# Performance work log

Measured on AMD Instinct MI355X. Metric: run time of the kernel, lower is better.

The kernel has to match this reference:

```python
import jax, jax.numpy as jnp
import numpy as np

B, TE, TD, DE, DD = 4, 256, 256, 512, 512


def setup_inputs() -> dict:
    key = jax.random.key(0)
    k1, k2, k3, k4, k5 = jax.random.split(key, 5)
    return {
        "encoder_outputs": jax.random.normal(k1, (B, TE, DE), dtype=jnp.float32),
        "decoder_outputs": jax.random.normal(k2, (B, TD, DD), dtype=jnp.float32),
        "U_a": jax.random.normal(k3, (DE, DE), dtype=jnp.float32) * 0.05,
        "W_a": jax.random.normal(k4, (DD, DE), dtype=jnp.float32) * 0.05,
        "V_a": jax.random.normal(k5, (DE,), dtype=jnp.float32) * 0.05,
    }


def reference(encoder_outputs, decoder_outputs, U_a, W_a, V_a):
    # U_a_dot_h: [B, Te, De] -- precomputed once, as in the original
    Uh = jnp.einsum("bec,cd->bed", encoder_outputs, U_a)
    # W_a_dot_s for all decoder steps at once (original loops over t): [B, Td, De]
    Ws = jnp.einsum("btc,cd->btd", decoder_outputs, W_a)
    # additive energies: tanh(Uh + Ws) . V_a -> [B, Td, Te]
    e = jnp.einsum("bted,d->bte", jnp.tanh(Uh[:, None, :, :] + Ws[:, :, None, :]), V_a)
    attn = jax.nn.softmax(e, axis=-1)  # softmax over encoder timesteps
    # context: weighted sum of encoder outputs -> [B, Td, De]
    context = jnp.einsum("bte,bec->btc", attn, encoder_outputs)
    return context, attn
```

## Files before the change

kernel.cpp:

```cpp
#include <hip/hip_runtime.h>

#define B_    4
#define TE_   256
#define TD_   256
#define DE_   512
#define K_    512

typedef __attribute__((ext_vector_type(8))) short bf16x8;
typedef __attribute__((ext_vector_type(4))) float f32x4;

#define C1F 2.8853900817779268f

__device__ __forceinline__ ushort f2bf(float x) {
  uint u = __float_as_uint(x);
  return (ushort)((u + 0x7fffu + ((u >> 16) & 1u)) >> 16);
}
__device__ __forceinline__ float bf2f(ushort h) {
  return __uint_as_float(((uint)h) << 16);
}
__device__ __forceinline__ float exp2_fast(float x) {
  float r;
  asm("v_exp_f32 %0, %1" : "=v"(r) : "v"(x));
  return r;
}

__global__ __launch_bounds__(256) void conv_hilo(
    const float* __restrict__ enc, const float* __restrict__ dec,
    ushort* __restrict__ ehi, ushort* __restrict__ elo,
    ushort* __restrict__ dhi, ushort* __restrict__ dlo) {
  const float* in = blockIdx.y ? dec : enc;
  ushort* hi = blockIdx.y ? dhi : ehi;
  ushort* lo = blockIdx.y ? dlo : elo;
  int i = (blockIdx.x * 256 + threadIdx.x) * 4;
  float4 v = *(const float4*)&in[i];
  ushort4 h, l;
  h.x = f2bf(v.x); l.x = f2bf(v.x - bf2f(h.x));
  h.y = f2bf(v.y); l.y = f2bf(v.y - bf2f(h.y));
  h.z = f2bf(v.z); l.z = f2bf(v.z - bf2f(h.z));
  h.w = f2bf(v.w); l.w = f2bf(v.w - bf2f(h.w));
  *(ushort4*)&hi[i] = h;
  *(ushort4*)&lo[i] = l;
}

__global__ __launch_bounds__(256) void conv_bt(
    const float* __restrict__ Ua, const float* __restrict__ Wa,
    ushort* __restrict__ uhi, ushort* __restrict__ ulo,
    ushort* __restrict__ whi, ushort* __restrict__ wlo) {
  const float* in = blockIdx.z ? Wa : Ua;
  ushort* thi = blockIdx.z ? whi : uhi;
  ushort* tlo = blockIdx.z ? wlo : ulo;
  __shared__ float tile[64][65];
  int k0 = blockIdx.y * 64, n0 = blockIdx.x * 64;
  int tid = threadIdx.x;
#pragma unroll
  for (int i = 0; i < 16; ++i) {
    int idx = tid + i * 256;
    int r = idx >> 6, c = idx & 63;
    tile[r][c] = in[(size_t)(k0 + r) * 512 + n0 + c];
  }
  __syncthreads();
#pragma unroll
  for (int i = 0; i < 16; ++i) {
    int idx = tid + i * 256;
    int rn = idx >> 6, ck = idx & 63;
    float x = tile[ck][rn] * C1F;
    ushort h = f2bf(x);
    size_t o = (size_t)(n0 + rn) * 512 + k0 + ck;
    thi[o] = h;
    tlo[o] = f2bf(x - bf2f(h));
  }
}

__global__ __launch_bounds__(64) void gemm_mfma(
    const ushort* __restrict__ ehi, const ushort* __restrict__ elo,
    const ushort* __restrict__ dhi, const ushort* __restrict__ dlo,
    const ushort* __restrict__ uhi, const ushort* __restrict__ ulo,
    const ushort* __restrict__ whi, const ushort* __restrict__ wlo,
    float* __restrict__ UhT, float* __restrict__ Ws) {
  const ushort *Ahi, *Alo, *Bhi, *Blo;
  int bid = blockIdx.x, bm, bn;
  if (blockIdx.z == 0) {
    Ahi = uhi; Alo = ulo; Bhi = ehi; Blo = elo;
    bn = (bid & 31) * 32; bm = (bid >> 5) * 32;
  } else {
    Ahi = dhi; Alo = dlo; Bhi = whi; Blo = wlo;
    bn = (bid & 15) * 32; bm = (bid >> 4) * 32;
  }
  int lane = threadIdx.x;
  int frow = lane & 15, fk = (lane >> 4) * 8;
  size_t ao = (size_t)(bm + frow) * K_ + fk;
  size_t bo = (size_t)(bn + frow) * K_ + fk;
  const ushort* pah0 = Ahi + ao; const ushort* pah1 = pah0 + 16 * K_;
  const ushort* pal0 = Alo + ao; const ushort* pal1 = pal0 + 16 * K_;
  const ushort* pbh0 = Bhi + bo; const ushort* pbh1 = pbh0 + 16 * K_;
  const ushort* pbl0 = Blo + bo; const ushort* pbl1 = pbl0 + 16 * K_;
  f32x4 a00 = {}, a01 = {}, a10 = {}, a11 = {};
#pragma unroll 2
  for (int k0 = 0; k0 < K_; k0 += 32) {
    bf16x8 ah0 = *(const bf16x8*)&pah0[k0], ah1 = *(const bf16x8*)&pah1[k0];
    bf16x8 al0 = *(const bf16x8*)&pal0[k0], al1 = *(const bf16x8*)&pal1[k0];
    bf16x8 bh0 = *(const bf16x8*)&pbh0[k0], bh1 = *(const bf16x8*)&pbh1[k0];
    bf16x8 bl0 = *(const bf16x8*)&pbl0[k0], bl1 = *(const bf16x8*)&pbl1[k0];
    a00 = __builtin_amdgcn_mfma_f32_16x16x32_bf16(ah0, bh0, a00, 0, 0, 0);
    a01 = __builtin_amdgcn_mfma_f32_16x16x32_bf16(ah0, bh1, a01, 0, 0, 0);
    a10 = __builtin_amdgcn_mfma_f32_16x16x32_bf16(ah1, bh0, a10, 0, 0, 0);
    a11 = __builtin_amdgcn_mfma_f32_16x16x32_bf16(ah1, bh1, a11, 0, 0, 0);
    a00 = __builtin_amdgcn_mfma_f32_16x16x32_bf16(ah0, bl0, a00, 0, 0, 0);
    a01 = __builtin_amdgcn_mfma_f32_16x16x32_bf16(ah0, bl1, a01, 0, 0, 0);
    a10 = __builtin_amdgcn_mfma_f32_16x16x32_bf16(ah1, bl0, a10, 0, 0, 0);
    a11 = __builtin_amdgcn_mfma_f32_16x16x32_bf16(ah1, bl1, a11, 0, 0, 0);
    a00 = __builtin_amdgcn_mfma_f32_16x16x32_bf16(al0, bh0, a00, 0, 0, 0);
    a01 = __builtin_amdgcn_mfma_f32_16x16x32_bf16(al0, bh1, a01, 0, 0, 0);
    a10 = __builtin_amdgcn_mfma_f32_16x16x32_bf16(al1, bh0, a10, 0, 0, 0);
    a11 = __builtin_amdgcn_mfma_f32_16x16x32_bf16(al1, bh1, a11, 0, 0, 0);
  }
  int crow = (lane >> 4) * 4, ccol = lane & 15;
#pragma unroll
  for (int i = 0; i < 2; ++i)
#pragma unroll
    for (int j = 0; j < 2; ++j) {
      const f32x4& acc = i == 0 ? (j == 0 ? a00 : a01) : (j == 0 ? a10 : a11);
      int m0 = bm + i * 16 + crow;
      int n0 = bn + j * 16 + ccol;
      if (blockIdx.z == 0) {
        float* cb = UhT + (size_t)(n0 >> 8) * 131072 + (size_t)m0 * 256 + (n0 & 255);
#pragma unroll
        for (int r = 0; r < 4; ++r) cb[(size_t)r * 256] = acc[r];
      } else {
        float* cb = Ws + (size_t)m0 * 512 + n0;
#pragma unroll
        for (int r = 0; r < 4; ++r) cb[(size_t)r * 512] = acc[r];
      }
    }
}

__global__ __launch_bounds__(512) void fused_attn(
    const float* __restrict__ enc, const float* __restrict__ UhT,
    const float* __restrict__ Ws, const float* __restrict__ Va,
    float* __restrict__ out_ctx, float* __restrict__ out_attn) {
  int bt = blockIdx.x;
  int b  = bt >> 7;
  int t0 = (bt & 127) * 2;
  __shared__ float ws0_s[520], ws1_s[520], mv_s[520];
  __shared__ float e_s[2][TE_];
  __shared__ float att2[TE_ * 2];
  __shared__ float redm[2][4], reds[2][4];
  int tid = threadIdx.x, lane = tid & 63, w = tid >> 6;

  const float* wsr = Ws + (size_t)(b * TD_ + t0) * DE_;
  int pd0 = tid + (tid >> 6);
  ws0_s[pd0] = wsr[tid];
  ws1_s[pd0] = wsr[DE_ + tid];
  mv_s[pd0]  = -2.0f * Va[tid];
  __syncthreads();

  int dg = lane >> 3, qlow = lane & 7;
  int q = w * 8 + qlow;
  const float* up = UhT + (size_t)b * 131072 + (size_t)dg * 64 * 256 + q * 4;
  int pbase = dg * 65;
  float a0[4] = {}, a1[4] = {};
#pragma unroll 8
  for (int i = 0; i < 64; ++i) {
    float4 u4 = *(const float4*)&up[(size_t)i * 256];
    float w0 = ws0_s[pbase + i];
    float w1 = ws1_s[pbase + i];
    float mv = mv_s[pbase + i];
#pragma unroll
    for (int j = 0; j < 4; ++j) {
      float u = j == 0 ? u4.x : j == 1 ? u4.y : j == 2 ? u4.z : u4.w;
      a0[j] = fmaf(mv, __builtin_amdgcn_rcpf(1.0f + exp2_fast(u + w0)), a0[j]);
      a1[j] = fmaf(mv, __builtin_amdgcn_rcpf(1.0f + exp2_fast(u + w1)), a1[j]);
    }
  }
#pragma unroll
  for (int j = 0; j < 4; ++j) {
#pragma unroll
    for (int off = 8; off <= 32; off <<= 1) {
      a0[j] += __shfl_xor(a0[j], off);
      a1[j] += __shfl_xor(a1[j], off);
    }
  }
  if (dg == 0) {
    float4 v0 = make_float4(a0[0], a0[1], a0[2], a0[3]);
    float4 v1 = make_float4(a1[0], a1[1], a1[2], a1[3]);
    *(float4*)&e_s[0][q * 4] = v0;
    *(float4*)&e_s[1][q * 4] = v1;
  }
  __syncthreads();

  int t = tid >> 8, col = tid & 255;
  float x = e_s[t][col];
  float m = x;
#pragma unroll
  for (int off = 32; off; off >>= 1) m = fmaxf(m, __shfl_xor(m, off));
  if (lane == 0) redm[t][w & 3] = m;
  __syncthreads();
  m = fmaxf(fmaxf(redm[t][0], redm[t][1]), fmaxf(redm[t][2], redm[t][3]));
  float p = __expf(x - m);
  float s = p;
#pragma unroll
  for (int off = 32; off; off >>= 1) s += __shfl_xor(s, off);
  if (lane == 0) reds[t][w & 3] = s;
  __syncthreads();
  s = reds[t][0] + reds[t][1] + reds[t][2] + reds[t][3];
  float a = p * __builtin_amdgcn_rcpf(s);
  att2[col * 2 + t] = a;
  out_attn[(size_t)(b * TD_ + t0 + t) * TE_ + col] = a;
  __syncthreads();

  const float* enc_b = enc + (size_t)b * TE_ * DE_;
  float c0 = 0.f, c1 = 0.f;
#pragma unroll 4
  for (int ee = 0; ee < TE_; ++ee) {
    float2 av = *(const float2*)&att2[ee * 2];
    float xv = enc_b[(size_t)ee * DE_ + tid];
    c0 = fmaf(av.x, xv, c0);
    c1 = fmaf(av.y, xv, c1);
  }
  float* ctx0 = out_ctx + (size_t)(b * TD_ + t0) * DE_;
  ctx0[tid]       = c0;
  ctx0[DE_ + tid] = c1;
}

extern "C" void kernel_launch(void* const* d_in, const int* in_sizes, int n_in,
                              void* d_out, int out_size, void* d_ws, size_t ws_size,
                              hipStream_t stream) {
  const float* enc = (const float*)d_in[0];
  const float* dec = (const float*)d_in[1];
  const float* Ua  = (const float*)d_in[2];
  const float* Wa  = (const float*)d_in[3];
  const float* Va  = (const float*)d_in[4];

  float* out_ctx  = (float*)d_out;
  float* out_attn = out_ctx + (size_t)B_ * TD_ * DE_;

  char* wsp = (char*)d_ws;
  float* UhT = (float*)wsp;             wsp += (size_t)B_ * DE_ * TE_ * 4;
  float* Wsm = (float*)wsp;             wsp += (size_t)B_ * TD_ * DE_ * 4;
  ushort* ehi = (ushort*)wsp;           wsp += (size_t)B_ * TE_ * DE_ * 2;
  ushort* elo = (ushort*)wsp;           wsp += (size_t)B_ * TE_ * DE_ * 2;
  ushort* dhi = (ushort*)wsp;           wsp += (size_t)B_ * TD_ * DE_ * 2;
  ushort* dlo = (ushort*)wsp;           wsp += (size_t)B_ * TD_ * DE_ * 2;
  ushort* uhi = (ushort*)wsp;           wsp += (size_t)K_ * DE_ * 2;
  ushort* ulo = (ushort*)wsp;           wsp += (size_t)K_ * DE_ * 2;
  ushort* whi = (ushort*)wsp;           wsp += (size_t)K_ * DE_ * 2;
  ushort* wlo = (ushort*)wsp;           wsp += (size_t)K_ * DE_ * 2;

  conv_hilo<<<dim3(512, 2), 256, 0, stream>>>(enc, dec, ehi, elo, dhi, dlo);
  conv_bt<<<dim3(8, 8, 2), 256, 0, stream>>>(Ua, Wa, uhi, ulo, whi, wlo);
  gemm_mfma<<<dim3(512, 1, 2), 64, 0, stream>>>(
      ehi, elo, dhi, dlo, uhi, ulo, whi, wlo, UhT, Wsm);
  fused_attn<<<512, 512, 0, stream>>>(enc, UhT, Wsm, Va, out_ctx, out_attn);
}
```

Measured before the change: 131.5 us.

## Merge conversion kernels, use 16x16 wave tiles in GEMM, double attention block threads

Merges the two bf16 hi/lo conversion kernels into one launch, removing one kernel launch. The GEMM now gives each wave a single 16x16 output tile, with four waves per block, instead of one 32x32 tile per single-wave block, which gives more waves for latency hiding. The fused attention kernel moves to 1024 threads per block, splitting the feature dimension across 16 waves and reducing partial energies through shared memory, and assigns one output row per thread in the context stage. The trade-offs are less register-level reuse of GEMM fragments, extra shared-memory reduction traffic, and higher per-block resource pressure.

```diff
diff --git a/kernel.cpp b/kernel.cpp
--- a/kernel.cpp
+++ b/kernel.cpp
@@ -24,34 +24,35 @@
   return r;
 }
 
-__global__ __launch_bounds__(256) void conv_hilo(
+__global__ __launch_bounds__(256) void conv_all(
     const float* __restrict__ enc, const float* __restrict__ dec,
+    const float* __restrict__ Ua, const float* __restrict__ Wa,
     ushort* __restrict__ ehi, ushort* __restrict__ elo,
-    ushort* __restrict__ dhi, ushort* __restrict__ dlo) {
-  const float* in = blockIdx.y ? dec : enc;
-  ushort* hi = blockIdx.y ? dhi : ehi;
-  ushort* lo = blockIdx.y ? dlo : elo;
-  int i = (blockIdx.x * 256 + threadIdx.x) * 4;
-  float4 v = *(const float4*)&in[i];
-  ushort4 h, l;
-  h.x = f2bf(v.x); l.x = f2bf(v.x - bf2f(h.x));
-  h.y = f2bf(v.y); l.y = f2bf(v.y - bf2f(h.y));
-  h.z = f2bf(v.z); l.z = f2bf(v.z - bf2f(h.z));
-  h.w = f2bf(v.w); l.w = f2bf(v.w - bf2f(h.w));
-  *(ushort4*)&hi[i] = h;
-  *(ushort4*)&lo[i] = l;
-}
-
-__global__ __launch_bounds__(256) void conv_bt(
-    const float* __restrict__ Ua, const float* __restrict__ Wa,
+    ushort* __restrict__ dhi, ushort* __restrict__ dlo,
     ushort* __restrict__ uhi, ushort* __restrict__ ulo,
     ushort* __restrict__ whi, ushort* __restrict__ wlo) {
-  const float* in = blockIdx.z ? Wa : Ua;
-  ushort* thi = blockIdx.z ? whi : uhi;
-  ushort* tlo = blockIdx.z ? wlo : ulo;
+  int z = blockIdx.z, tid = threadIdx.x;
+  if (z < 2) {
+    const float* in = z ? dec : enc;
+    ushort* hi = z ? dhi : ehi;
+    ushort* lo = z ? dlo : elo;
+    int i = (blockIdx.x * 256 + tid) * 4;
+    float4 v = *(const float4*)&in[i];
+    ushort4 h, l;
+    h.x = f2bf(v.x); l.x = f2bf(v.x - bf2f(h.x));
+    h.y = f2bf(v.y); l.y = f2bf(v.y - bf2f(h.y));
+    h.z = f2bf(v.z); l.z = f2bf(v.z - bf2f(h.z));
+    h.w = f2bf(v.w); l.w = f2bf(v.w - bf2f(h.w));
+    *(ushort4*)&hi[i] = h;
+    *(ushort4*)&lo[i] = l;
+    return;
+  }
+  if (blockIdx.x >= 64) return;
+  const float* in = (z == 3) ? Wa : Ua;
+  ushort* thi = (z == 3) ? whi : uhi;
+  ushort* tlo = (z == 3) ? wlo : ulo;
   __shared__ float tile[64][65];
-  int k0 = blockIdx.y * 64, n0 = blockIdx.x * 64;
-  int tid = threadIdx.x;
+  int k0 = (blockIdx.x >> 3) * 64, n0 = (blockIdx.x & 7) * 64;
 #pragma unroll
   for (int i = 0; i < 16; ++i) {
     int idx = tid + i * 256;
@@ -71,70 +72,55 @@
   }
 }
 
-__global__ __launch_bounds__(64) void gemm_mfma(
+__global__ __launch_bounds__(256, 4) void gemm_mfma(
     const ushort* __restrict__ ehi, const ushort* __restrict__ elo,
     const ushort* __restrict__ dhi, const ushort* __restrict__ dlo,
     const ushort* __restrict__ uhi, const ushort* __restrict__ ulo,
     const ushort* __restrict__ whi, const ushort* __restrict__ wlo,
     float* __restrict__ UhT, float* __restrict__ Ws) {
   const ushort *Ahi, *Alo, *Bhi, *Blo;
-  int bid = blockIdx.x, bm, bn;
+  int tid = threadIdx.x, lane = tid & 63;
+  int ti = blockIdx.x * 4 + (tid >> 6);
+  int bm, bn;
   if (blockIdx.z == 0) {
     Ahi = uhi; Alo = ulo; Bhi = ehi; Blo = elo;
-    bn = (bid & 31) * 32; bm = (bid >> 5) * 32;
+    bm = (ti >> 6) * 16; bn = (ti & 63) * 16;
   } else {
     Ahi = dhi; Alo = dlo; Bhi = whi; Blo = wlo;
-    bn = (bid & 15) * 32; bm = (bid >> 4) * 32;
-  }
-  int lane = threadIdx.x;
+    bm = (ti >> 5) * 16; bn = (ti & 31) * 16;
+  }
   int frow = lane & 15, fk = (lane >> 4) * 8;
   size_t ao = (size_t)(bm + frow) * K_ + fk;
   size_t bo = (size_t)(bn + frow) * K_ + fk;
-  const ushort* pah0 = Ahi + ao; const ushort* pah1 = pah0 + 16 * K_;
-  const ushort* pal0 = Alo + ao; const ushort* pal1 = pal0 + 16 * K_;
-  const ushort* pbh0 = Bhi + bo; const ushort* pbh1 = pbh0 + 16 * K_;
-  const ushort* pbl0 = Blo + bo; const ushort* pbl1 = pbl0 + 16 * K_;
-  f32x4 a00 = {}, a01 = {}, a10 = {}, a11 = {};
-#pragma unroll 2
+  const ushort* pah = Ahi + ao;
+  const ushort* pal = Alo + ao;
+  const ushort* pbh = Bhi + bo;
+  const ushort* pbl = Blo + bo;
+  f32x4 acc = {};
+#pragma unroll 4
   for (int k0 = 0; k0 < K_; k0 += 32) {
-    bf16x8 ah0 = *(const bf16x8*)&pah0[k0], ah1 = *(const bf16x8*)&pah1[k0];
-    bf16x8 al0 = *(const bf16x8*)&pal0[k0], al1 = *(const bf16x8*)&pal1[k0];
-    bf16x8 bh0 = *(const bf16x8*)&pbh0[k0], bh1 = *(const bf16x8*)&pbh1[k0];
-    bf16x8 bl0 = *(const bf16x8*)&pbl0[k0], bl1 = *(const bf16x8*)&pbl1[k0];
-    a00 = __builtin_amdgcn_mfma_f32_16x16x32_bf16(ah0, bh0, a00, 0, 0, 0);
-    a01 = __builtin_amdgcn_mfma_f32_16x16x32_bf16(ah0, bh1, a01, 0, 0, 0);
-    a10 = __builtin_amdgcn_mfma_f32_16x16x32_bf16(ah1, bh0, a10, 0, 0, 0);
-    a11 = __builtin_amdgcn_mfma_f32_16x16x32_bf16(ah1, bh1, a11, 0, 0, 0);
-    a00 = __builtin_amdgcn_mfma_f32_16x16x32_bf16(ah0, bl0, a00, 0, 0, 0);
-    a01 = __builtin_amdgcn_mfma_f32_16x16x32_bf16(ah0, bl1, a01, 0, 0, 0);
-    a10 = __builtin_amdgcn_mfma_f32_16x16x32_bf16(ah1, bl0, a10, 0, 0, 0);
-    a11 = __builtin_amdgcn_mfma_f32_16x16x32_bf16(ah1, bl1, a11, 0, 0, 0);
-    a00 = __builtin_amdgcn_mfma_f32_16x16x32_bf16(al0, bh0, a00, 0, 0, 0);
-    a01 = __builtin_amdgcn_mfma_f32_16x16x32_bf16(al0, bh1, a01, 0, 0, 0);
-    a10 = __builtin_amdgcn_mfma_f32_16x16x32_bf16(al1, bh0, a10, 0, 0, 0);
-    a11 = __builtin_amdgcn_mfma_f32_16x16x32_bf16(al1, bh1, a11, 0, 0, 0);
-  }
-  int crow = (lane >> 4) * 4, ccol = lane & 15;
-#pragma unroll
-  for (int i = 0; i < 2; ++i)
-#pragma unroll
-    for (int j = 0; j < 2; ++j) {
-      const f32x4& acc = i == 0 ? (j == 0 ? a00 : a01) : (j == 0 ? a10 : a11);
-      int m0 = bm + i * 16 + crow;
-      int n0 = bn + j * 16 + ccol;
-      if (blockIdx.z == 0) {
-        float* cb = UhT + (size_t)(n0 >> 8) * 131072 + (size_t)m0 * 256 + (n0 & 255);
-#pragma unroll
-        for (int r = 0; r < 4; ++r) cb[(size_t)r * 256] = acc[r];
-      } else {
-        float* cb = Ws + (size_t)m0 * 512 + n0;
-#pragma unroll
-        for (int r = 0; r < 4; ++r) cb[(size_t)r * 512] = acc[r];
-      }
-    }
-}
-
-__global__ __launch_bounds__(512) void fused_attn(
+    bf16x8 ah = *(const bf16x8*)&pah[k0];
+    bf16x8 al = *(const bf16x8*)&pal[k0];
+    bf16x8 bh = *(const bf16x8*)&pbh[k0];
+    bf16x8 bl = *(const bf16x8*)&pbl[k0];
+    acc = __builtin_amdgcn_mfma_f32_16x16x32_bf16(ah, bh, acc, 0, 0, 0);
+    acc = __builtin_amdgcn_mfma_f32_16x16x32_bf16(ah, bl, acc, 0, 0, 0);
+    acc = __builtin_amdgcn_mfma_f32_16x16x32_bf16(al, bh, acc, 0, 0, 0);
+  }
+  int m0 = bm + (lane >> 4) * 4;
+  int n0 = bn + (lane & 15);
+  if (blockIdx.z == 0) {
+    float* cb = UhT + (size_t)(n0 >> 8) * 131072 + (size_t)m0 * 256 + (n0 & 255);
+#pragma unroll
+    for (int r = 0; r < 4; ++r) cb[(size_t)r * 256] = acc[r];
+  } else {
+    float* cb = Ws + (size_t)m0 * 512 + n0;
+#pragma unroll
+    for (int r = 0; r < 4; ++r) cb[(size_t)r * 512] = acc[r];
+  }
+}
+
+__global__ __launch_bounds__(1024, 8) void fused_attn(
     const float* __restrict__ enc, const float* __restrict__ UhT,
     const float* __restrict__ Ws, const float* __restrict__ Va,
     float* __restrict__ out_ctx, float* __restrict__ out_attn) {
@@ -142,29 +128,27 @@
   int b  = bt >> 7;
   int t0 = (bt & 127) * 2;
   __shared__ float ws0_s[520], ws1_s[520], mv_s[520];
-  __shared__ float e_s[2][TE_];
+  __shared__ float part[32][260];
   __shared__ float att2[TE_ * 2];
   __shared__ float redm[2][4], reds[2][4];
   int tid = threadIdx.x, lane = tid & 63, w = tid >> 6;
 
-  const float* wsr = Ws + (size_t)(b * TD_ + t0) * DE_;
-  int pd0 = tid + (tid >> 6);
-  ws0_s[pd0] = wsr[tid];
-  ws1_s[pd0] = wsr[DE_ + tid];
-  mv_s[pd0]  = -2.0f * Va[tid];
-  __syncthreads();
-
-  int dg = lane >> 3, qlow = lane & 7;
-  int q = w * 8 + qlow;
-  const float* up = UhT + (size_t)b * 131072 + (size_t)dg * 64 * 256 + q * 4;
-  int pbase = dg * 65;
+  if (tid < 512) {
+    const float* wsr = Ws + (size_t)(b * TD_ + t0) * DE_;
+    int pd = tid + (tid >> 6);
+    ws0_s[pd] = wsr[tid];
+    ws1_s[pd] = wsr[DE_ + tid];
+    mv_s[pd]  = -2.0f * Va[tid];
+  }
+  __syncthreads();
+
+  const float* up = UhT + (size_t)b * 131072 + (size_t)w * 32 * 256 + lane * 4;
   float a0[4] = {}, a1[4] = {};
-#pragma unroll 8
-  for (int i = 0; i < 64; ++i) {
-    float4 u4 = *(const float4*)&up[(size_t)i * 256];
-    float w0 = ws0_s[pbase + i];
-    float w1 = ws1_s[pbase + i];
-    float mv = mv_s[pbase + i];
+#pragma unroll 4
+  for (int row = 0; row < 32; ++row) {
+    float4 u4 = *(const float4*)&up[row * 256];
+    int d = w * 32 + row, pd = d + (d >> 6);
+    float w0 = ws0_s[pd], w1 = ws1_s[pd], mv = mv_s[pd];
 #pragma unroll
     for (int j = 0; j < 4; ++j) {
       float u = j == 0 ? u4.x : j == 1 ? u4.y : j == 2 ? u4.z : u4.w;
@@ -172,54 +156,45 @@
       a1[j] = fmaf(mv, __builtin_amdgcn_rcpf(1.0f + exp2_fast(u + w1)), a1[j]);
     }
   }
-#pragma unroll
-  for (int j = 0; j < 4; ++j) {
-#pragma unroll
-    for (int off = 8; off <= 32; off <<= 1) {
-      a0[j] += __shfl_xor(a0[j], off);
-      a1[j] += __shfl_xor(a1[j], off);
-    }
-  }
-  if (dg == 0) {
-    float4 v0 = make_float4(a0[0], a0[1], a0[2], a0[3]);
-    float4 v1 = make_float4(a1[0], a1[1], a1[2], a1[3]);
-    *(float4*)&e_s[0][q * 4] = v0;
-    *(float4*)&e_s[1][q * 4] = v1;
-  }
+  *(float4*)&part[w * 2 + 0][lane * 4] = make_float4(a0[0], a0[1], a0[2], a0[3]);
+  *(float4*)&part[w * 2 + 1][lane * 4] = make_float4(a1[0], a1[1], a1[2], a1[3]);
   __syncthreads();
 
   int t = tid >> 8, col = tid & 255;
-  float x = e_s[t][col];
-  float m = x;
-#pragma unroll
-  for (int off = 32; off; off >>= 1) m = fmaxf(m, __shfl_xor(m, off));
-  if (lane == 0) redm[t][w & 3] = m;
-  __syncthreads();
-  m = fmaxf(fmaxf(redm[t][0], redm[t][1]), fmaxf(redm[t][2], redm[t][3]));
-  float p = __expf(x - m);
-  float s = p;
-#pragma unroll
-  for (int off = 32; off; off >>= 1) s += __shfl_xor(s, off);
-  if (lane == 0) reds[t][w & 3] = s;
-  __syncthreads();
-  s = reds[t][0] + reds[t][1] + reds[t][2] + reds[t][3];
-  float a = p * __builtin_amdgcn_rcpf(s);
-  att2[col * 2 + t] = a;
-  out_attn[(size_t)(b * TD_ + t0 + t) * TE_ + col] = a;
-  __syncthreads();
-
+  float x = 0.f, p = 0.f, m, s;
+  if (tid < 512) {
+#pragma unroll
+    for (int ww = 0; ww < 16; ++ww) x += part[ww * 2 + t][col];
+    m = x;
+#pragma unroll
+    for (int off = 32; off; off >>= 1) m = fmaxf(m, __shfl_xor(m, off));
+    if (lane == 0) redm[t][w & 3] = m;
+  }
+  __syncthreads();
+  if (tid < 512) {
+    m = fmaxf(fmaxf(redm[t][0], redm[t][1]), fmaxf(redm[t][2], redm[t][3]));
+    p = __expf(x - m);
+    s = p;
+#pragma unroll
+    for (int off = 32; off; off >>= 1) s += __shfl_xor(s, off);
+    if (lane == 0) reds[t][w & 3] = s;
+  }
+  __syncthreads();
+  if (tid < 512) {
+    s = reds[t][0] + reds[t][1] + reds[t][2] + reds[t][3];
+    float a = p * __builtin_amdgcn_rcpf(s);
+    att2[col * 2 + t] = a;
+    out_attn[(size_t)(b * TD_ + t0 + t) * TE_ + col] = a;
+  }
+  __syncthreads();
+
+  int d = tid & 511, tt = tid >> 9;
   const float* enc_b = enc + (size_t)b * TE_ * DE_;
-  float c0 = 0.f, c1 = 0.f;
+  float c = 0.f;
 #pragma unroll 4
-  for (int ee = 0; ee < TE_; ++ee) {
-    float2 av = *(const float2*)&att2[ee * 2];
-    float xv = enc_b[(size_t)ee * DE_ + tid];
-    c0 = fmaf(av.x, xv, c0);
-    c1 = fmaf(av.y, xv, c1);
-  }
-  float* ctx0 = out_ctx + (size_t)(b * TD_ + t0) * DE_;
-  ctx0[tid]       = c0;
-  ctx0[DE_ + tid] = c1;
+  for (int ee = 0; ee < TE_; ++ee)
+    c = fmaf(att2[ee * 2 + tt], enc_b[(size_t)ee * DE_ + d], c);
+  out_ctx[(size_t)(b * TD_ + t0 + tt) * DE_ + d] = c;
 }
 
 extern "C" void kernel_launch(void* const* d_in, const int* in_sizes, int n_in,
@@ -246,9 +221,9 @@
   ushort* whi = (ushort*)wsp;           wsp += (size_t)K_ * DE_ * 2;
   ushort* wlo = (ushort*)wsp;           wsp += (size_t)K_ * DE_ * 2;
 
-  conv_hilo<<<dim3(512, 2), 256, 0, stream>>>(enc, dec, ehi, elo, dhi, dlo);
-  conv_bt<<<dim3(8, 8, 2), 256, 0, stream>>>(Ua, Wa, uhi, ulo, whi, wlo);
-  gemm_mfma<<<dim3(512, 1, 2), 64, 0, stream>>>(
+  conv_all<<<dim3(512, 1, 4), 256, 0, stream>>>(
+      enc, dec, Ua, Wa, ehi, elo, dhi, dlo, uhi, ulo, whi, wlo);
+  gemm_mfma<<<dim3(512, 1, 2), 256, 0, stream>>>(
       ehi, elo, dhi, dlo, uhi, ulo, whi, wlo, UhT, Wsm);
-  fused_attn<<<512, 512, 0, stream>>>(enc, UhT, Wsm, Va, out_ctx, out_attn);
-}
+  fused_attn<<<512, 1024, 0, stream>>>(enc, UhT, Wsm, Va, out_ctx, out_attn);
+}
```

New measurement: 144.5 us. 9.8% more time.
